# Optimization experiments

Hardware: AMD Instinct MI355X
Metric: run time of the kernel (lower is better)

Reference implementation:

```python
import jax, jax.numpy as jnp
import numpy as np

B, N, D, H, A = 4, 512, 128, 64, 100

def _ln(x, g, eps=1e-5):
    # LayerNorm with bias=False (weight only), biased variance like torch
    m = jnp.mean(x, axis=-1, keepdims=True)
    v = jnp.var(x, axis=-1, keepdims=True)
    return (x - m) * jax.lax.rsqrt(v + eps) * g

def setup_inputs() -> dict:
    key = jax.random.key(0)
    ks = jax.random.split(key, 16)
    s = 0.05
    return {
        "atoms": jax.random.randint(ks[0], (B, N), 0, A),
        "rel_dist": jax.random.uniform(ks[1], (B, N, N), dtype=jnp.float32),
        "adj_mat": jax.random.randint(ks[2], (B, N, N), 0, 2).astype(bool),
        "mask": jnp.ones((B, N), dtype=bool),
        "radius_cutoff_softmask": jax.random.uniform(ks[3], (B, N, N), dtype=jnp.float32),
        # embeddings
        "atom_tab": jax.random.normal(ks[4], (A, D), jnp.float32) * s,
        "neigh_tab": jax.random.normal(ks[5], (A, D), jnp.float32) * s,
        # radial MLP: Linear(1,H) SiLU LN(H) Linear(H,H) SiLU LN(H) Linear(H,D)
        "rW1": jax.random.normal(ks[6], (1, H), jnp.float32) * s,
        "rb1": jnp.zeros((H,), jnp.float32),
        "rg1": jnp.ones((H,), jnp.float32),
        "rW2": jax.random.normal(ks[7], (H, H), jnp.float32) * s,
        "rb2": jnp.zeros((H,), jnp.float32),
        "rg2": jnp.ones((H,), jnp.float32),
        "rW3": jax.random.normal(ks[8], (H, D), jnp.float32) * s,
        "rb3": jnp.zeros((D,), jnp.float32),
        # to_node_feats: Linear(2D,D) LN(D) SiLU Linear(D,D)
        "nW1": jax.random.normal(ks[9], (2 * D, D), jnp.float32) * s,
        "nb1": jnp.zeros((D,), jnp.float32),
        "ng": jnp.ones((D,), jnp.float32),
        "nW2": jax.random.normal(ks[10], (D, D), jnp.float32) * s,
        "nb2": jnp.zeros((D,), jnp.float32),
    }

def reference(atoms, rel_dist, adj_mat, mask, radius_cutoff_softmask,
              atom_tab, neigh_tab,
              rW1, rb1, rg1, rW2, rb2, rg2, rW3, rb3,
              nW1, nb1, ng, nW2, nb2):
    dtype = rel_dist.dtype
    eye = jnp.eye(N, dtype=bool)
    adj = (adj_mat & ~eye).astype(dtype)                     # [b,n,n]

    embeds = atom_tab[atoms]                                 # [b,n,d]
    neighbor_embeds = neigh_tab[atoms]                       # [b,n,d]

    # radial MLP on pairwise distances -> [b,n,n,d]
    h = jax.nn.silu(rel_dist[..., None] @ rW1 + rb1)         # [b,n,n,H]
    h = _ln(h, rg1)
    h = _ln(jax.nn.silu(h @ rW2 + rb2), rg2)
    feats = h @ rW3 + rb3                                    # [b,n,n,d]

    feats = jnp.where(mask[:, None, :, None], feats, jnp.zeros((), dtype))
    feats = feats * radius_cutoff_softmask[..., None]

    neighbor_feats = jnp.einsum('bij,bijd,bjd->bid', adj, feats, neighbor_embeds)

    x = jnp.concatenate([embeds, neighbor_feats], axis=-1)   # [b,n,2d]
    x = jax.nn.silu(_ln(x @ nW1 + nb1, ng))
    return x @ nW2 + nb2                                     # [b,n,d]
```

## Files before the change

### kernel.cpp

```cpp
#include <hip/hip_runtime.h>
#include <hip/hip_bf16.h>
#include <math.h>

#define Bn 4
#define Nn 512
#define Dn 128
#define Hn 64
#define TT 4096
#define EPB 8
#define K0B ((TT + 1 + EPB - 1) / EPB)

__device__ __forceinline__ float silu_f(float x) {
    return x * (1.0f / (1.0f + __expf(-x)));
}

struct K0S {
    float rW2s[Hn][Hn];
    float rW3s[Hn][Dn];
    float rW1s[Hn], rb1s[Hn], rg1s[Hn], rb2s[Hn], rg2s[Hn];
    float rb3s[Dn];
    float h1buf[4][Hn];
    float h2buf[4][Hn];
};

__global__ __launch_bounds__(256)
void k0_build_table(const float* __restrict__ rW1, const float* __restrict__ rb1,
                    const float* __restrict__ rg1,
                    const float* __restrict__ rW2, const float* __restrict__ rb2,
                    const float* __restrict__ rg2,
                    const float* __restrict__ rW3, const float* __restrict__ rb3,
                    __hip_bfloat16* __restrict__ table)
{
    __shared__ K0S sm;
    const int t   = threadIdx.x;
    const int k   = t & 63;
    const int wv  = t >> 6;
    const int blk = blockIdx.x;

    #pragma unroll
    for (int idx = t; idx < Hn * Hn; idx += 256)
        sm.rW2s[idx >> 6][idx & 63] = rW2[idx];
    #pragma unroll
    for (int idx = t; idx < Hn * Dn; idx += 256)
        sm.rW3s[idx >> 7][idx & 127] = rW3[idx];
    if (t < Hn) {
        sm.rW1s[t] = rW1[t];
        sm.rb1s[t] = rb1[t];
        sm.rg1s[t] = rg1[t];
        sm.rb2s[t] = rb2[t];
        sm.rg2s[t] = rg2[t];
    }
    if (t < Dn) sm.rb3s[t] = rb3[t];
    __syncthreads();

    for (int r = 0; r < 2; ++r) {
        const int e = blk * EPB + r * 4 + wv;
        const float x = (float)e * (1.0f / (float)TT);

        float h = silu_f(x * sm.rW1s[k] + sm.rb1s[k]);
        float s1 = h, s2 = h * h;
        #pragma unroll
        for (int m = 1; m < 64; m <<= 1) { s1 += __shfl_xor(s1, m); s2 += __shfl_xor(s2, m); }
        float mean = s1 * (1.0f / 64.0f);
        float var  = s2 * (1.0f / 64.0f) - mean * mean;
        float rs   = rsqrtf(var + 1e-5f);
        sm.h1buf[wv][k] = (h - mean) * rs * sm.rg1s[k];
        __syncthreads();

        float p = 0.f;
        #pragma unroll 8
        for (int kk = 0; kk < Hn; ++kk) p += sm.h1buf[wv][kk] * sm.rW2s[kk][k];
        float h2 = silu_f(p + sm.rb2s[k]);
        s1 = h2; s2 = h2 * h2;
        #pragma unroll
        for (int m = 1; m < 64; m <<= 1) { s1 += __shfl_xor(s1, m); s2 += __shfl_xor(s2, m); }
        mean = s1 * (1.0f / 64.0f);
        var  = s2 * (1.0f / 64.0f) - mean * mean;
        rs   = rsqrtf(var + 1e-5f);
        sm.h2buf[wv][k] = (h2 - mean) * rs * sm.rg2s[k];
        __syncthreads();

        #pragma unroll
        for (int dd = 0; dd < 2; ++dd) {
            const int d = dd * 64 + k;
            float f = sm.rb3s[d];
            #pragma unroll 8
            for (int kk = 0; kk < Hn; ++kk) f += sm.h2buf[wv][kk] * sm.rW3s[kk][d];
            if (e <= TT) table[e * Dn + d] = __float2bfloat16(f);
        }
        __syncthreads();
    }
}

struct K1S {
    __hip_bfloat162 ntabS[100 * 64];
    union {
        float2 ent[4][512];
        struct {
            float xs[4][256];
            float pp[8][4][128];
            float sarr[4][128];
            float x2[4][128];
            float st1[4], st2[4];
        } epi;
    } u;
    float accs[4][2][32][4];
};

__global__ __launch_bounds__(256)
void k1_fused(const int* __restrict__ atoms, const float* __restrict__ rel,
              const int* __restrict__ adj, const int* __restrict__ mask,
              const float* __restrict__ soft, const float* __restrict__ ntab,
              const __hip_bfloat16* __restrict__ table,
              const float* __restrict__ atom_tab,
              const float* __restrict__ nW1, const float* __restrict__ nb1,
              const float* __restrict__ ng,
              const float* __restrict__ nW2, const float* __restrict__ nb2,
              float* __restrict__ out)
{
    __shared__ K1S sm;
    const int t    = threadIdx.x;
    const int lane = t & 63;
    const int wv   = t >> 6;
    const int bi0  = blockIdx.x * 4;
    const int b    = bi0 >> 9;

    for (int idx = t; idx < 100 * 64; idx += 256) {
        const float2 fv = ((const float2*)ntab)[idx];
        sm.ntabS[idx] = __hip_bfloat162(__float2bfloat16(fv.x), __float2bfloat16(fv.y));
    }

    const int ig      = bi0 + wv;
    const int iloc    = ig & 511;
    const int rowbase = ig * Nn;
    const unsigned long long below = (1ull << lane) - 1ull;

    int cnt = 0;
    #pragma unroll
    for (int c = 0; c < 8; ++c) {
        const int j = c * 64 + lane;
        const float dist = rel[rowbase + j];
        const int   adjv = adj[rowbase + j];
        const int   mk   = mask[b * Nn + j];
        const float w = (adjv != 0 && mk != 0 && j != iloc) ? soft[rowbase + j] : 0.0f;
        int e = (int)(dist * (float)TT + 0.5f);
        e = min(max(e, 0), TT);
        const bool act = (w != 0.0f);
        const unsigned long long bm = __ballot(act);
        const int pre = __popcll(bm & below);
        if (act) sm.u.ent[wv][cnt + pre] =
            make_float2(w, __int_as_float(e | (atoms[b * Nn + j] << 16)));
        cnt += (int)__popcll(bm);
    }
    const int padded = (cnt + 7) & ~7;
    if (lane < padded - cnt)
        sm.u.ent[wv][cnt + lane] = make_float2(0.0f, __int_as_float(0));
    __syncthreads();

    const int s  = lane >> 5;
    const int dl = lane & 31;
    const int d0 = dl * 4;
    float a0 = 0.f, a1 = 0.f, a2 = 0.f, a3 = 0.f;
    #pragma unroll 8
    for (int n = s; n < padded; n += 2) {
        const float2 E  = sm.u.ent[wv][n];
        const float w   = E.x;
        const int  meta = __float_as_int(E.y);
        const int  e    = meta & 0xFFFF;
        const int  at   = meta >> 16;
        const __hip_bfloat162* tp = (const __hip_bfloat162*)&table[e * Dn + d0];
        const __hip_bfloat162 tva = tp[0], tvb = tp[1];
        const __hip_bfloat162 nva = sm.ntabS[at * 64 + dl * 2];
        const __hip_bfloat162 nvb = sm.ntabS[at * 64 + dl * 2 + 1];
        const float2 ta = __bfloat1622float2(tva);
        const float2 tb = __bfloat1622float2(tvb);
        const float2 na = __bfloat1622float2(nva);
        const float2 nb = __bfloat1622float2(nvb);
        a0 += (w * na.x) * ta.x;
        a1 += (w * na.y) * ta.y;
        a2 += (w * nb.x) * tb.x;
        a3 += (w * nb.y) * tb.y;
    }
    *(float4*)&sm.accs[wv][s][dl][0] = make_float4(a0, a1, a2, a3);
    __syncthreads();

    const int og = t & 31;
    const int ch = t >> 5;

    #pragma unroll
    for (int idx = t; idx < 4 * 256; idx += 256) {
        const int r = idx >> 8, c = idx & 255;
        float v;
        if (c < Dn) {
            v = atom_tab[atoms[bi0 + r] * Dn + c];
        } else {
            const int d  = c - Dn;
            v = sm.accs[r][0][d >> 2][d & 3] + sm.accs[r][1][d >> 2][d & 3];
        }
        sm.u.epi.xs[r][c] = v;
    }
    __syncthreads();

    {
        float acc[4][4];
        #pragma unroll
        for (int r = 0; r < 4; ++r)
            #pragma unroll
            for (int k = 0; k < 4; ++k) acc[r][k] = 0.f;
        const int c0 = ch * 32;
        #pragma unroll 8
        for (int c = 0; c < 32; ++c) {
            const float4 wv4 = *(const float4*)&nW1[(c0 + c) * Dn + og * 4];
            #pragma unroll
            for (int r = 0; r < 4; ++r) {
                const float xv = sm.u.epi.xs[r][c0 + c];
                acc[r][0] += xv * wv4.x; acc[r][1] += xv * wv4.y;
                acc[r][2] += xv * wv4.z; acc[r][3] += xv * wv4.w;
            }
        }
        #pragma unroll
        for (int r = 0; r < 4; ++r)
            *(float4*)&sm.u.epi.pp[ch][r][og * 4] =
                make_float4(acc[r][0], acc[r][1], acc[r][2], acc[r][3]);
    }
    __syncthreads();

    if (t < Dn) {
        #pragma unroll
        for (int r = 0; r < 4; ++r) {
            float sv = nb1[t];
            #pragma unroll
            for (int cc = 0; cc < 8; ++cc) sv += sm.u.epi.pp[cc][r][t];
            sm.u.epi.sarr[r][t] = sv;
        }
    }
    __syncthreads();

    {
        const float va = sm.u.epi.sarr[wv][lane];
        const float vb = sm.u.epi.sarr[wv][lane + 64];
        float s1 = va + vb, s2 = va * va + vb * vb;
        #pragma unroll
        for (int m = 1; m < 64; m <<= 1) { s1 += __shfl_xor(s1, m); s2 += __shfl_xor(s2, m); }
        if (lane == 0) { sm.u.epi.st1[wv] = s1; sm.u.epi.st2[wv] = s2; }
    }
    __syncthreads();

    {
        const int r0 = t >> 7, d = t & 127;
        const float gd = ng[d];
        #pragma unroll
        for (int q = 0; q < 2; ++q) {
            const int r = r0 + 2 * q;
            const float m  = sm.u.epi.st1[r] * (1.0f / 128.0f);
            const float vr = sm.u.epi.st2[r] * (1.0f / 128.0f) - m * m;
            const float rs = rsqrtf(vr + 1e-5f);
            sm.u.epi.x2[r][d] = silu_f((sm.u.epi.sarr[r][d] - m) * rs * gd);
        }
    }
    __syncthreads();

    {
        float acc[4][4];
        #pragma unroll
        for (int r = 0; r < 4; ++r)
            #pragma unroll
            for (int k = 0; k < 4; ++k) acc[r][k] = 0.f;
        const int c0 = ch * 16;
        #pragma unroll
        for (int c = 0; c < 16; ++c) {
            const float4 wv4 = *(const float4*)&nW2[(c0 + c) * Dn + og * 4];
            #pragma unroll
            for (int r = 0; r < 4; ++r) {
                const float xv = sm.u.epi.x2[r][c0 + c];
                acc[r][0] += xv * wv4.x; acc[r][1] += xv * wv4.y;
                acc[r][2] += xv * wv4.z; acc[r][3] += xv * wv4.w;
            }
        }
        #pragma unroll
        for (int r = 0; r < 4; ++r)
            *(float4*)&sm.u.epi.pp[ch][r][og * 4] =
                make_float4(acc[r][0], acc[r][1], acc[r][2], acc[r][3]);
    }
    __syncthreads();

    if (t < Dn) {
        #pragma unroll
        for (int r = 0; r < 4; ++r) {
            float sv = nb2[t];
            #pragma unroll
            for (int cc = 0; cc < 8; ++cc) sv += sm.u.epi.pp[cc][r][t];
            out[(bi0 + r) * Dn + t] = sv;
        }
    }
}

extern "C" void kernel_launch(void* const* d_in, const int* in_sizes, int n_in,
                              void* d_out, int out_size, void* d_ws, size_t ws_size,
                              hipStream_t stream)
{
    (void)in_sizes; (void)n_in; (void)out_size; (void)ws_size;

    const int*   atoms = (const int*)d_in[0];
    const float* rel   = (const float*)d_in[1];
    const int*   adj   = (const int*)d_in[2];
    const int*   mask  = (const int*)d_in[3];
    const float* soft  = (const float*)d_in[4];
    const float* atab  = (const float*)d_in[5];
    const float* ntab  = (const float*)d_in[6];
    const float* rW1   = (const float*)d_in[7];
    const float* rb1   = (const float*)d_in[8];
    const float* rg1   = (const float*)d_in[9];
    const float* rW2   = (const float*)d_in[10];
    const float* rb2   = (const float*)d_in[11];
    const float* rg2   = (const float*)d_in[12];
    const float* rW3   = (const float*)d_in[13];
    const float* rb3   = (const float*)d_in[14];
    const float* nW1   = (const float*)d_in[15];
    const float* nb1   = (const float*)d_in[16];
    const float* ng    = (const float*)d_in[17];
    const float* nW2   = (const float*)d_in[18];
    const float* nb2   = (const float*)d_in[19];

    __hip_bfloat16* table = (__hip_bfloat16*)d_ws;
    float* out = (float*)d_out;

    hipLaunchKernelGGL(k0_build_table, dim3(K0B), dim3(256), 0, stream,
                       rW1, rb1, rg1, rW2, rb2, rg2, rW3, rb3, table);
    hipLaunchKernelGGL(k1_fused, dim3(Bn * Nn / 4), dim3(256), 0, stream,
                       atoms, rel, adj, mask, soft, ntab, table,
                       atab, nW1, nb1, ng, nW2, nb2, out);
}
```

Baseline: 138.0 us.

## Use wave shuffles instead of shared buffers and barriers in both kernels

In the table-building kernel, the shared-memory h1/h2 buffers and their block barriers are replaced with in-wave __shfl broadcasts, and each block now builds twice as many table entries (EPB 16). In the fused kernel, the gather loop uses 16-byte bf16 loads with 8 accumulators per lane, and the partial sums are reduced with xor-shuffles instead of a shared accs array. The embedding is preloaded early, and the LayerNorm epilogue runs one row per wave, which removes several barriers and shared-memory passes. The cost is higher register pressure, fewer blocks in the first kernel, and four-way striding over neighbours, which can leave lanes idle when a row has few neighbours.

```diff
diff --git a/kernel.cpp b/kernel.cpp
--- a/kernel.cpp
+++ b/kernel.cpp
@@ -7,7 +7,7 @@
 #define Dn 128
 #define Hn 64
 #define TT 4096
-#define EPB 8
+#define EPB 16
 #define K0B ((TT + 1 + EPB - 1) / EPB)
 
 __device__ __forceinline__ float silu_f(float x) {
@@ -19,8 +19,6 @@
     float rW3s[Hn][Dn];
     float rW1s[Hn], rb1s[Hn], rg1s[Hn], rb2s[Hn], rg2s[Hn];
     float rb3s[Dn];
-    float h1buf[4][Hn];
-    float h2buf[4][Hn];
 };
 
 __global__ __launch_bounds__(256)
@@ -32,10 +30,9 @@
                     __hip_bfloat16* __restrict__ table)
 {
     __shared__ K0S sm;
-    const int t   = threadIdx.x;
-    const int k   = t & 63;
-    const int wv  = t >> 6;
-    const int blk = blockIdx.x;
+    const int t  = threadIdx.x;
+    const int k  = t & 63;
+    const int wv = t >> 6;
 
     #pragma unroll
     for (int idx = t; idx < Hn * Hn; idx += 256)
@@ -53,42 +50,44 @@
     if (t < Dn) sm.rb3s[t] = rb3[t];
     __syncthreads();
 
-    for (int r = 0; r < 2; ++r) {
-        const int e = blk * EPB + r * 4 + wv;
+    const float w1v = sm.rW1s[k], b1v = sm.rb1s[k], g1v = sm.rg1s[k];
+    const float b2v = sm.rb2s[k], g2v = sm.rg2s[k];
+
+    for (int r = 0; r < EPB / 4; ++r) {
+        const int e = blockIdx.x * EPB + r * 4 + wv;
         const float x = (float)e * (1.0f / (float)TT);
 
-        float h = silu_f(x * sm.rW1s[k] + sm.rb1s[k]);
+        float h = silu_f(x * w1v + b1v);
         float s1 = h, s2 = h * h;
         #pragma unroll
         for (int m = 1; m < 64; m <<= 1) { s1 += __shfl_xor(s1, m); s2 += __shfl_xor(s2, m); }
         float mean = s1 * (1.0f / 64.0f);
         float var  = s2 * (1.0f / 64.0f) - mean * mean;
-        float rs   = rsqrtf(var + 1e-5f);
-        sm.h1buf[wv][k] = (h - mean) * rs * sm.rg1s[k];
-        __syncthreads();
+        const float h1n = (h - mean) * rsqrtf(var + 1e-5f) * g1v;
 
         float p = 0.f;
-        #pragma unroll 8
-        for (int kk = 0; kk < Hn; ++kk) p += sm.h1buf[wv][kk] * sm.rW2s[kk][k];
-        float h2 = silu_f(p + sm.rb2s[k]);
+        #pragma unroll
+        for (int kk = 0; kk < Hn; ++kk)
+            p += __shfl(h1n, kk) * sm.rW2s[kk][k];
+        float h2 = silu_f(p + b2v);
         s1 = h2; s2 = h2 * h2;
         #pragma unroll
         for (int m = 1; m < 64; m <<= 1) { s1 += __shfl_xor(s1, m); s2 += __shfl_xor(s2, m); }
         mean = s1 * (1.0f / 64.0f);
         var  = s2 * (1.0f / 64.0f) - mean * mean;
-        rs   = rsqrtf(var + 1e-5f);
-        sm.h2buf[wv][k] = (h2 - mean) * rs * sm.rg2s[k];
-        __syncthreads();
-
-        #pragma unroll
-        for (int dd = 0; dd < 2; ++dd) {
-            const int d = dd * 64 + k;
-            float f = sm.rb3s[d];
-            #pragma unroll 8
-            for (int kk = 0; kk < Hn; ++kk) f += sm.h2buf[wv][kk] * sm.rW3s[kk][d];
-            if (e <= TT) table[e * Dn + d] = __float2bfloat16(f);
-        }
-        __syncthreads();
+        const float h2n = (h2 - mean) * rsqrtf(var + 1e-5f) * g2v;
+
+        float f0 = sm.rb3s[k], f1 = sm.rb3s[64 + k];
+        #pragma unroll
+        for (int kk = 0; kk < Hn; ++kk) {
+            const float hb = __shfl(h2n, kk);
+            f0 += hb * sm.rW3s[kk][k];
+            f1 += hb * sm.rW3s[kk][64 + k];
+        }
+        if (e <= TT) {
+            table[e * Dn + k]      = __float2bfloat16(f0);
+            table[e * Dn + 64 + k] = __float2bfloat16(f1);
+        }
     }
 }
 
@@ -99,12 +98,9 @@
         struct {
             float xs[4][256];
             float pp[8][4][128];
-            float sarr[4][128];
             float x2[4][128];
-            float st1[4], st2[4];
         } epi;
     } u;
-    float accs[4][2][32][4];
 };
 
 __global__ __launch_bounds__(256)
@@ -135,6 +131,8 @@
     const int rowbase = ig * Nn;
     const unsigned long long below = (1ull << lane) - 1ull;
 
+    const float2 embv = ((const float2*)&atom_tab[atoms[ig] * Dn])[lane];
+
     int cnt = 0;
     #pragma unroll
     for (int c = 0; c < 8; ++c) {
@@ -157,56 +155,60 @@
         sm.u.ent[wv][cnt + lane] = make_float2(0.0f, __int_as_float(0));
     __syncthreads();
 
-    const int s  = lane >> 5;
-    const int dl = lane & 31;
-    const int d0 = dl * 4;
+    const int s  = lane >> 4;
+    const int dl = lane & 15;
+    const int d0 = dl * 8;
     float a0 = 0.f, a1 = 0.f, a2 = 0.f, a3 = 0.f;
+    float a4 = 0.f, a5 = 0.f, a6 = 0.f, a7 = 0.f;
     #pragma unroll 8
-    for (int n = s; n < padded; n += 2) {
+    for (int n = s; n < padded; n += 4) {
         const float2 E  = sm.u.ent[wv][n];
         const float w   = E.x;
         const int  meta = __float_as_int(E.y);
         const int  e    = meta & 0xFFFF;
         const int  at   = meta >> 16;
-        const __hip_bfloat162* tp = (const __hip_bfloat162*)&table[e * Dn + d0];
-        const __hip_bfloat162 tva = tp[0], tvb = tp[1];
-        const __hip_bfloat162 nva = sm.ntabS[at * 64 + dl * 2];
-        const __hip_bfloat162 nvb = sm.ntabS[at * 64 + dl * 2 + 1];
-        const float2 ta = __bfloat1622float2(tva);
-        const float2 tb = __bfloat1622float2(tvb);
-        const float2 na = __bfloat1622float2(nva);
-        const float2 nb = __bfloat1622float2(nvb);
-        a0 += (w * na.x) * ta.x;
-        a1 += (w * na.y) * ta.y;
-        a2 += (w * nb.x) * tb.x;
-        a3 += (w * nb.y) * tb.y;
-    }
-    *(float4*)&sm.accs[wv][s][dl][0] = make_float4(a0, a1, a2, a3);
+        union { float4 f; __hip_bfloat162 h[4]; } T, Nv;
+        T.f  = *(const float4*)&table[e * Dn + d0];
+        Nv.f = *(const float4*)&sm.ntabS[at * 64 + dl * 4];
+        const float2 t0 = __bfloat1622float2(T.h[0]);
+        const float2 t1 = __bfloat1622float2(T.h[1]);
+        const float2 t2 = __bfloat1622float2(T.h[2]);
+        const float2 t3 = __bfloat1622float2(T.h[3]);
+        const float2 n0 = __bfloat1622float2(Nv.h[0]);
+        const float2 n1 = __bfloat1622float2(Nv.h[1]);
+        const float2 n2 = __bfloat1622float2(Nv.h[2]);
+        const float2 n3 = __bfloat1622float2(Nv.h[3]);
+        a0 += (w * n0.x) * t0.x;  a1 += (w * n0.y) * t0.y;
+        a2 += (w * n1.x) * t1.x;  a3 += (w * n1.y) * t1.y;
+        a4 += (w * n2.x) * t2.x;  a5 += (w * n2.y) * t2.y;
+        a6 += (w * n3.x) * t3.x;  a7 += (w * n3.y) * t3.y;
+    }
+    a0 += __shfl_xor(a0, 16); a1 += __shfl_xor(a1, 16);
+    a2 += __shfl_xor(a2, 16); a3 += __shfl_xor(a3, 16);
+    a4 += __shfl_xor(a4, 16); a5 += __shfl_xor(a5, 16);
+    a6 += __shfl_xor(a6, 16); a7 += __shfl_xor(a7, 16);
+    a0 += __shfl_xor(a0, 32); a1 += __shfl_xor(a1, 32);
+    a2 += __shfl_xor(a2, 32); a3 += __shfl_xor(a3, 32);
+    a4 += __shfl_xor(a4, 32); a5 += __shfl_xor(a5, 32);
+    a6 += __shfl_xor(a6, 32); a7 += __shfl_xor(a7, 32);
+    __syncthreads();
+
+    ((float2*)&sm.u.epi.xs[wv][0])[lane] = embv;
+    if (lane < 16) {
+        *(float4*)&sm.u.epi.xs[wv][Dn + d0]     = make_float4(a0, a1, a2, a3);
+        *(float4*)&sm.u.epi.xs[wv][Dn + d0 + 4] = make_float4(a4, a5, a6, a7);
+    }
     __syncthreads();
 
     const int og = t & 31;
     const int ch = t >> 5;
 
-    #pragma unroll
-    for (int idx = t; idx < 4 * 256; idx += 256) {
-        const int r = idx >> 8, c = idx & 255;
-        float v;
-        if (c < Dn) {
-            v = atom_tab[atoms[bi0 + r] * Dn + c];
-        } else {
-            const int d  = c - Dn;
-            v = sm.accs[r][0][d >> 2][d & 3] + sm.accs[r][1][d >> 2][d & 3];
-        }
-        sm.u.epi.xs[r][c] = v;
-    }
-    __syncthreads();
-
     {
         float acc[4][4];
         #pragma unroll
         for (int r = 0; r < 4; ++r)
             #pragma unroll
-            for (int k = 0; k < 4; ++k) acc[r][k] = 0.f;
+            for (int q = 0; q < 4; ++q) acc[r][q] = 0.f;
         const int c0 = ch * 32;
         #pragma unroll 8
         for (int c = 0; c < 32; ++c) {
@@ -225,38 +227,21 @@
     }
     __syncthreads();
 
-    if (t < Dn) {
-        #pragma unroll
-        for (int r = 0; r < 4; ++r) {
-            float sv = nb1[t];
-            #pragma unroll
-            for (int cc = 0; cc < 8; ++cc) sv += sm.u.epi.pp[cc][r][t];
-            sm.u.epi.sarr[r][t] = sv;
-        }
-    }
-    __syncthreads();
-
     {
-        const float va = sm.u.epi.sarr[wv][lane];
-        const float vb = sm.u.epi.sarr[wv][lane + 64];
-        float s1 = va + vb, s2 = va * va + vb * vb;
+        float lo = nb1[lane], hi = nb1[lane + 64];
+        #pragma unroll
+        for (int cc = 0; cc < 8; ++cc) {
+            lo += sm.u.epi.pp[cc][wv][lane];
+            hi += sm.u.epi.pp[cc][wv][lane + 64];
+        }
+        float s1 = lo + hi, s2 = lo * lo + hi * hi;
         #pragma unroll
         for (int m = 1; m < 64; m <<= 1) { s1 += __shfl_xor(s1, m); s2 += __shfl_xor(s2, m); }
-        if (lane == 0) { sm.u.epi.st1[wv] = s1; sm.u.epi.st2[wv] = s2; }
-    }
-    __syncthreads();
-
-    {
-        const int r0 = t >> 7, d = t & 127;
-        const float gd = ng[d];
-        #pragma unroll
-        for (int q = 0; q < 2; ++q) {
-            const int r = r0 + 2 * q;
-            const float m  = sm.u.epi.st1[r] * (1.0f / 128.0f);
-            const float vr = sm.u.epi.st2[r] * (1.0f / 128.0f) - m * m;
-            const float rs = rsqrtf(vr + 1e-5f);
-            sm.u.epi.x2[r][d] = silu_f((sm.u.epi.sarr[r][d] - m) * rs * gd);
-        }
+        const float mean = s1 * (1.0f / 128.0f);
+        const float var  = s2 * (1.0f / 128.0f) - mean * mean;
+        const float rs   = rsqrtf(var + 1e-5f);
+        sm.u.epi.x2[wv][lane]      = silu_f((lo - mean) * rs * ng[lane]);
+        sm.u.epi.x2[wv][lane + 64] = silu_f((hi - mean) * rs * ng[lane + 64]);
     }
     __syncthreads();
 
@@ -265,7 +250,7 @@
         #pragma unroll
         for (int r = 0; r < 4; ++r)
             #pragma unroll
-            for (int k = 0; k < 4; ++k) acc[r][k] = 0.f;
+            for (int q = 0; q < 4; ++q) acc[r][q] = 0.f;
         const int c0 = ch * 16;
         #pragma unroll
         for (int c = 0; c < 16; ++c) {
@@ -284,14 +269,15 @@
     }
     __syncthreads();
 
-    if (t < Dn) {
-        #pragma unroll
-        for (int r = 0; r < 4; ++r) {
-            float sv = nb2[t];
-            #pragma unroll
-            for (int cc = 0; cc < 8; ++cc) sv += sm.u.epi.pp[cc][r][t];
-            out[(bi0 + r) * Dn + t] = sv;
-        }
+    {
+        float lo = nb2[lane], hi = nb2[lane + 64];
+        #pragma unroll
+        for (int cc = 0; cc < 8; ++cc) {
+            lo += sm.u.epi.pp[cc][wv][lane];
+            hi += sm.u.epi.pp[cc][wv][lane + 64];
+        }
+        out[(bi0 + wv) * Dn + lane]      = lo;
+        out[(bi0 + wv) * Dn + lane + 64] = hi;
     }
 }
 
```

New measurement: 147.9 us. 7.2% more time.
